# Optimization experiments

Hardware: AMD Instinct MI355X
Metric: run time of the kernel (lower is better)

## Reference

```python
import jax, jax.numpy as jnp
import numpy as np

HIDDEN = 512
HEADS = 8
HEAD_DIM = HIDDEN // HEADS  # 64
NUM_FEATURES = 256
EPS = 1e-4


def _gaussian_orthogonal_random_matrix(num_rows, num_cols, scaling=0, seed=1234):
    """Blocks of orthogonal rows from QR of gaussian matrices, rescaled (FAVOR+)."""
    rng = np.random.default_rng(seed)
    blocks = []
    full_blocks = num_rows // num_cols
    for _ in range(full_blocks):
        q, _ = np.linalg.qr(rng.standard_normal((num_cols, num_cols)))
        blocks.append(q.T)
    rem = num_rows - full_blocks * num_cols
    if rem > 0:
        q, _ = np.linalg.qr(rng.standard_normal((num_cols, num_cols)))
        blocks.append(q.T[:rem])
    mat = np.concatenate(blocks, axis=0)  # [num_rows, num_cols]
    if scaling == 0:
        # row norms of a fresh gaussian matrix (chi-distributed multipliers)
        multiplier = np.linalg.norm(rng.standard_normal((num_rows, num_cols)), axis=1)
    else:
        multiplier = np.sqrt(num_cols) * np.ones(num_rows)
    return (multiplier[:, None] * mat).astype(np.float32)


def _split_heads(x, b):
    # [b, n, hidden] -> [b, h, n, head_dim]
    return x.reshape(b, -1, HEADS, HEAD_DIM).transpose(0, 2, 1, 3)


def _phi(data, proj):
    """Nonnegative softmax kernel feature map (FAVOR+).
    data: [b,h,n,d], proj: [m,d] -> [b,h,n,m]"""
    d = data.shape[-1]
    m = proj.shape[0]
    x = data * (d ** -0.25)
    dash = jnp.einsum('bhnd,md->bhnm', x, proj)
    diag = 0.5 * jnp.sum(x * x, axis=-1, keepdims=True)
    return (m ** -0.5) * jnp.exp(dash - diag) + EPS


def setup_inputs() -> dict:
    key = jax.random.key(0)
    ks = jax.random.split(key, 12)
    b, n = 2, 8192
    s = HIDDEN ** -0.5
    inp = {
        'query': jax.random.normal(ks[0], (b, n, HIDDEN), jnp.float32),
        'key':   jax.random.normal(ks[1], (b, n, HIDDEN), jnp.float32),
        'value': jax.random.normal(ks[2], (b, n, HIDDEN), jnp.float32),
        'WQ_w': jax.random.normal(ks[3], (HIDDEN, HIDDEN), jnp.float32) * s,
        'WQ_b': jnp.zeros((HIDDEN,), jnp.float32),
        'WK_w': jax.random.normal(ks[4], (HIDDEN, HIDDEN), jnp.float32) * s,
        'WK_b': jnp.zeros((HIDDEN,), jnp.float32),
        'WV_w': jax.random.normal(ks[5], (HIDDEN, HIDDEN), jnp.float32) * s,
        'WV_b': jnp.zeros((HIDDEN,), jnp.float32),
        'WO_w': jax.random.normal(ks[6], (HIDDEN, HIDDEN), jnp.float32) * s,
        'WO_b': jnp.zeros((HIDDEN,), jnp.float32),
        'proj': jnp.asarray(_gaussian_orthogonal_random_matrix(NUM_FEATURES, HEAD_DIM)),
    }
    return inp


def reference(query, key, value, WQ_w, WQ_b, WK_w, WK_b, WV_w, WV_b, WO_w, WO_b, proj):
    b = query.shape[0]
    # torch Linear: y = x @ W.T + b
    Q = _split_heads(jnp.einsum('bnd,ed->bne', query, WQ_w) + WQ_b, b)
    K = _split_heads(jnp.einsum('bnd,ed->bne', key,   WK_w) + WK_b, b)
    V = _split_heads(jnp.einsum('bnd,ed->bne', value, WV_w) + WV_b, b)

    Qp = _phi(Q, proj)  # [b,h,n,m]
    Kp = _phi(K, proj)  # [b,h,n,m]

    # denominator: Q' @ sum_n K'  -> [b,h,n,1]
    denom = jnp.einsum('bhnm,bhm->bhn', Qp, jnp.sum(Kp, axis=2))[..., None]
    # linear attention: Q' @ (K'^T V), O(n*m*d)
    ctx = jnp.einsum('bhnm,bhnd->bhmd', Kp, V)
    attn = jnp.einsum('bhnm,bhmd->bhnd', Qp, ctx) / denom

    # faithful to original: .view(batch, -1, hidden) directly on [b,h,n,d]
    attn = attn.reshape(b, -1, HIDDEN)
    return jnp.einsum('bnd,ed->bne', attn, WO_w) + WO_b
```

## Files before the change

### kernel.cpp

```cpp
#include <hip/hip_runtime.h>

typedef __attribute__((ext_vector_type(8))) _Float16 f16x8;
typedef __attribute__((ext_vector_type(4))) float f32x4;

#define S4 0.35355339059327373f

static __device__ __forceinline__ ushort f2h(float f) {
  return __builtin_bit_cast(ushort, (_Float16)f);
}

static __device__ __forceinline__ void gload16(const void* g, void* l) {
  __builtin_amdgcn_global_load_lds((const __attribute__((address_space(1))) void*)g,
                                   (__attribute__((address_space(3))) void*)l, 16, 0, 0);
}

static __device__ __forceinline__ void cvt_store8(ushort* dst, float4 a, float4 b) {
  f16x8 h;
  h[0] = (_Float16)a.x; h[1] = (_Float16)a.y; h[2] = (_Float16)a.z; h[3] = (_Float16)a.w;
  h[4] = (_Float16)b.x; h[5] = (_Float16)b.y; h[6] = (_Float16)b.z; h[7] = (_Float16)b.w;
  *(f16x8*)dst = h;
}

template<int BM, int BN, int WR, int WC, int EPI, int ZMODE, int DIAG, int AF32, int BF32>
__global__ __launch_bounds__(256) void gemm_bt(
    const void* __restrict__ Av, const void* __restrict__ Bv,
    const float* __restrict__ bias, ushort* __restrict__ Cb,
    float* __restrict__ Cf, const float* __restrict__ rv0,
    float* __restrict__ dg,
    int K, int ldA, int ldB, int ldC, int Mz,
    long sAz, long sBz, long sCz)
{
  constexpr int BK = 32;
  constexpr int WTM = BM / WR, WTN = BN / WC;
  constexpr int MI = WTM / 16, NI = WTN / 16;
  constexpr int LDSB = (BM + BN) * 64;

  __shared__ uint4 smem4[LDSB / 16];
  char* smem = (char*)smem4;
  ushort* As = (ushort*)smem;
  ushort* Bs = (ushort*)(smem + BM * 64);

  const int tid = threadIdx.x;
  const int l = tid & 63, w = tid >> 6;
  const int wr = w / WC, wc = w % WC;
  const int lr = l & 15, lk = l >> 4;
  const int tm = blockIdx.x * BM, tn = blockIdx.y * BN;
  const int z = blockIdx.z;

  const ushort* Ah = (const ushort*)Av;
  const ushort* Bh = (const ushort*)Bv;
  const float*  Af = (const float*)Av;
  const float*  Bf = (const float*)Bv;
  long aoff = 0, boff = 0;
  if (ZMODE == 0) { aoff = (long)z * sAz; boff = (long)z * sBz; }
  if (ZMODE == 2) { aoff = (long)z * sAz; boff = (long)(z >> 3) * sBz + (z & 7) * 64; }
  if (ZMODE == 3) {
    aoff = (long)(z & 15) * sAz + (long)(z >> 4) * 1024;
    boff = (long)(z & 15) * sBz + (long)(z >> 4) * 1024;
  }
  Ah += aoff; Bh += boff; Af += aoff; Bf += boff;
  const float* rv = (EPI == 6) ? (rv0 + (long)z * Mz) : nullptr;
  const long coff = (long)z * sCz;

  f32x4 acc[MI][NI];
#pragma unroll
  for (int i = 0; i < MI; ++i)
#pragma unroll
    for (int j = 0; j < NI; ++j) acc[i][j] = f32x4{0.f, 0.f, 0.f, 0.f};

  for (int k0 = 0; k0 < K; k0 += BK) {
    if constexpr (AF32) {
      const int ar = tid >> 1, ac = (tid & 1) * 16;
      const float* g = Af + (long)(tm + ar) * ldA + k0 + ac;
      float4 f0 = *(const float4*)(g);
      float4 f1 = *(const float4*)(g + 4);
      float4 f2 = *(const float4*)(g + 8);
      float4 f3 = *(const float4*)(g + 12);
      cvt_store8(As + ar * 32 + ac, f0, f1);
      cvt_store8(As + ar * 32 + ac + 8, f2, f3);
    } else {
      constexpr int AB = BM * 64;
#pragma unroll
      for (int s = 0; s < (AB + 4095) / 4096; ++s) {
        const int base = s * 4096 + w * 1024;
        if (base < AB) {
          const int idx = base + l * 16;
          gload16(Ah + (long)(tm + (idx >> 6)) * ldA + k0 + ((idx & 63) >> 1),
                  (char*)As + base);
        }
      }
    }
    if constexpr (BF32) {
      const int br = tid >> 1, bc = (tid & 1) * 16;
      const float* g = Bf + (long)(tn + br) * ldB + k0 + bc;
      float4 f0 = *(const float4*)(g);
      float4 f1 = *(const float4*)(g + 4);
      float4 f2 = *(const float4*)(g + 8);
      float4 f3 = *(const float4*)(g + 12);
      cvt_store8(Bs + br * 32 + bc, f0, f1);
      cvt_store8(Bs + br * 32 + bc + 8, f2, f3);
    } else {
      constexpr int BB = BN * 64;
#pragma unroll
      for (int s = 0; s < (BB + 4095) / 4096; ++s) {
        const int base = s * 4096 + w * 1024;
        if (base < BB) {
          const int idx = base + l * 16;
          gload16(Bh + (long)(tn + (idx >> 6)) * ldB + k0 + ((idx & 63) >> 1),
                  (char*)Bs + base);
        }
      }
    }
    __syncthreads();

    f16x8 af[MI], bfr[NI];
#pragma unroll
    for (int mi = 0; mi < MI; ++mi)
      af[mi] = *(const f16x8*)(As + (wr * WTM + mi * 16 + lr) * 32 + lk * 8);
#pragma unroll
    for (int ni = 0; ni < NI; ++ni)
      bfr[ni] = *(const f16x8*)(Bs + (wc * WTN + ni * 16 + lr) * 32 + lk * 8);
#pragma unroll
    for (int mi = 0; mi < MI; ++mi)
#pragma unroll
      for (int ni = 0; ni < NI; ++ni)
        acc[mi][ni] = __builtin_amdgcn_mfma_f32_16x16x32_f16(af[mi], bfr[ni], acc[mi][ni], 0, 0, 0);
    __syncthreads();
  }

#pragma unroll
  for (int mi = 0; mi < MI; ++mi) {
#pragma unroll
    for (int j = 0; j < 4; ++j) {
      const int row = tm + wr * WTM + mi * 16 + lk * 4 + j;
      float ds = 0.f;
#pragma unroll
      for (int ni = 0; ni < NI; ++ni) {
        const int col = tn + wc * WTN + ni * 16 + lr;
        float v = acc[mi][ni][j];
        if (EPI == 0 || EPI == 3) v += bias[col];
        if (EPI == 4) v += bias[row];
        if (EPI == 6) v = 0.0625f * __expf(v - rv[col]) + 1e-4f;
        if (DIAG) ds += v * v;
        if (EPI == 4) {
          const int b = col >> 13, nn = col & 8191;
          const int h = row >> 6, d = row & 63;
          Cb[(long)(b * 8 + h) * 655360 + (long)d * 8192 + nn] = f2h(v);
        } else if (EPI == 3 || EPI == 5) {
          Cf[coff + (long)row * ldC + col] = v;
        } else {
          Cb[coff + (long)row * ldC + col] = f2h(v);
        }
      }
      if (DIAG) {
        ds += __shfl_xor(ds, 1, 64);
        ds += __shfl_xor(ds, 2, 64);
        ds += __shfl_xor(ds, 4, 64);
        ds += __shfl_xor(ds, 8, 64);
        if (lr == 0) {
          const int b = row >> 13, nn = row & 8191;
          const int head = (tn + wc * WTN) >> 6;
          dg[(long)(b * 8 + head) * 8192 + nn] = 0.0625f * ds;
        }
      }
    }
  }
}

__global__ __launch_bounds__(256) void phiattn_k(
    const ushort* __restrict__ Qh, const ushort* __restrict__ pjh,
    const float* __restrict__ diagQ, const ushort* __restrict__ ctxb,
    ushort* __restrict__ attnR)
{
  const int bx = blockIdx.x, bh = blockIdx.y;
  const int b = bh >> 3, h = bh & 7;
  const int tm = bx * 64;
  const int tid = threadIdx.x, l = tid & 63, w = tid >> 6;
  const int lr = l & 15, lk = l >> 4;

  __shared__ char smem[46080];
  ushort* P  = (ushort*)smem;
  ushort* As = (ushort*)(smem + 33792);
  ushort* Bs = (ushort*)(smem + 37888);

  const ushort* QB = Qh + (long)b * 4194304 + h * 64;
  const float* rv = diagQ + (long)bh * 8192;

  for (int nh = 0; nh < 2; ++nh) {
    const ushort* PB = pjh + nh * 8192;
    f32x4 a2[8];
#pragma unroll
    for (int i = 0; i < 8; ++i) a2[i] = f32x4{0.f, 0.f, 0.f, 0.f};

    for (int k0 = 0; k0 < 64; k0 += 32) {
      {
        const int base = w * 1024;
        const int idx = base + l * 16;
        gload16(QB + (long)(tm + (idx >> 6)) * 512 + k0 + ((idx & 63) >> 1),
                (char*)As + base);
      }
#pragma unroll
      for (int s = 0; s < 2; ++s) {
        const int base = s * 4096 + w * 1024;
        const int idx = base + l * 16;
        gload16(PB + (long)(idx >> 6) * 64 + k0 + ((idx & 63) >> 1),
                (char*)Bs + base);
      }
      __syncthreads();
      f16x8 af = *(const f16x8*)(As + (w * 16 + lr) * 32 + lk * 8);
#pragma unroll
      for (int ni = 0; ni < 8; ++ni) {
        f16x8 bfr = *(const f16x8*)(Bs + (ni * 16 + lr) * 32 + lk * 8);
        a2[ni] = __builtin_amdgcn_mfma_f32_16x16x32_f16(af, bfr, a2[ni], 0, 0, 0);
      }
      __syncthreads();
    }
#pragma unroll
    for (int ni = 0; ni < 8; ++ni)
#pragma unroll
      for (int j = 0; j < 4; ++j) {
        const int row = w * 16 + lk * 4 + j;
        const int col = nh * 128 + ni * 16 + lr;
        const float vv = 0.0625f * __expf(a2[ni][j] - rv[tm + row]) + 1e-4f;
        P[row * 264 + col] = f2h(vv);
      }
  }
  __syncthreads();

  f32x4 acc[5];
#pragma unroll
  for (int i = 0; i < 5; ++i) acc[i] = f32x4{0.f, 0.f, 0.f, 0.f};

  const ushort* cb = ctxb + (long)bh * 20480;
  for (int k0 = 0; k0 < 256; k0 += 32) {
    f16x8 pa = *(const f16x8*)(P + (w * 16 + lr) * 264 + k0 + lk * 8);
#pragma unroll
    for (int ni = 0; ni < 5; ++ni) {
      f16x8 cf = *(const f16x8*)(cb + (long)(ni * 16 + lr) * 256 + k0 + lk * 8);
      acc[ni] = __builtin_amdgcn_mfma_f32_16x16x32_f16(pa, cf, acc[ni], 0, 0, 0);
    }
  }

  ushort* outb = attnR + (long)bh * 524288;
#pragma unroll
  for (int j = 0; j < 4; ++j) {
    const float dv = __shfl(acc[4][j], (l & 48), 64);
    const int row = tm + w * 16 + lk * 4 + j;
#pragma unroll
    for (int ni = 0; ni < 4; ++ni) {
      const int col = ni * 16 + lr;
      outb[(long)row * 64 + col] = f2h(acc[ni][j] / dv);
    }
  }
}

__global__ __launch_bounds__(256) void cvtall_k(
    const float* __restrict__ wq, const float* __restrict__ wk,
    const float* __restrict__ wv, const float* __restrict__ wo,
    const float* __restrict__ pj,
    ushort* __restrict__ wqh, ushort* __restrict__ wkh,
    ushort* __restrict__ wvh, ushort* __restrict__ woh,
    ushort* __restrict__ pjh)
{
  int i = blockIdx.x * 256 + threadIdx.x;
  const float* in; ushort* out; float scale = 1.f; int idx;
  if (i < 65536)       { in = wq; out = wqh; idx = i; }
  else if (i < 131072) { in = wk; out = wkh; idx = i - 65536; }
  else if (i < 196608) { in = wv; out = wvh; idx = i - 131072; }
  else if (i < 262144) { in = wo; out = woh; idx = i - 196608; }
  else if (i < 266240) { in = pj; out = pjh; idx = i - 262144; scale = S4; }
  else return;
  float4 v = ((const float4*)in)[idx];
  ushort4 o;
  o.x = f2h(v.x * scale); o.y = f2h(v.y * scale);
  o.z = f2h(v.z * scale); o.w = f2h(v.w * scale);
  ((ushort4*)out)[idx] = o;
}

__global__ __launch_bounds__(256) void vtpad_k(ushort* __restrict__ Vt) {
  const int i = blockIdx.x * 256 + threadIdx.x;
  const int bh = i >> 14, rem = i & 16383, r = rem >> 10, n8 = rem & 1023;
  const unsigned val = (r == 0) ? 0x3C003C00u : 0u;
  uint4 u; u.x = val; u.y = val; u.z = val; u.w = val;
  *(uint4*)(Vt + (long)bh * 655360 + (long)(64 + r) * 8192 + n8 * 8) = u;
}

__global__ __launch_bounds__(256) void ctxred_k(const float* __restrict__ cp,
                                                ushort* __restrict__ ctxb) {
  const int idx = blockIdx.x * 256 + threadIdx.x;
  const int bh = idx / 20480, rem = idx % 20480;
  float a = 0.f;
#pragma unroll
  for (int kc = 0; kc < 8; ++kc) a += cp[(long)(kc * 16 + bh) * 20480 + rem];
  ctxb[idx] = f2h(a);
}

extern "C" void kernel_launch(void* const* d_in, const int* in_sizes, int n_in,
                              void* d_out, int out_size, void* d_ws, size_t ws_size,
                              hipStream_t stream) {
  (void)in_sizes; (void)n_in; (void)out_size; (void)ws_size;
  const float* q  = (const float*)d_in[0];
  const float* k  = (const float*)d_in[1];
  const float* v  = (const float*)d_in[2];
  const float* wq = (const float*)d_in[3];
  const float* bq = (const float*)d_in[4];
  const float* wk = (const float*)d_in[5];
  const float* bk = (const float*)d_in[6];
  const float* wv = (const float*)d_in[7];
  const float* bv = (const float*)d_in[8];
  const float* wo = (const float*)d_in[9];
  const float* bo = (const float*)d_in[10];
  const float* pj = (const float*)d_in[11];

  char* ws = (char*)d_ws;
  ushort* attnR = (ushort*)(ws + 0);
  float*  cpart = (float*)(ws + 16777216);
  ushort* wqh   = (ushort*)(ws + 27262976);
  ushort* wkh   = (ushort*)(ws + 27787264);
  ushort* wvh   = (ushort*)(ws + 28311552);
  ushort* woh   = (ushort*)(ws + 28835840);
  ushort* pjh   = (ushort*)(ws + 29360128);
  ushort* Qh    = (ushort*)(ws + 29392896);
  ushort* Kh    = (ushort*)(ws + 46170112);
  ushort* Vt    = (ushort*)(ws + 62947328);
  ushort* KpT   = (ushort*)(ws + 83918848);
  float*  diagQ = (float*)(ws + 151027712);
  float*  diagK = (float*)(ws + 151552000);
  ushort* ctxb  = (ushort*)(ws + 152076288);

  cvtall_k<<<1040, 256, 0, stream>>>(wq, wk, wv, wo, pj, wqh, wkh, wvh, woh, pjh);
  vtpad_k<<<1024, 256, 0, stream>>>(Vt);

  gemm_bt<128,128,2,2,0,0,1,1,0><<<dim3(128,4,1), 256, 0, stream>>>(
      q, wqh, bq, Qh, nullptr, nullptr, diagQ, 512, 512, 512, 512, 0, 0L, 0L, 0L);
  gemm_bt<128,128,2,2,0,0,1,1,0><<<dim3(128,4,1), 256, 0, stream>>>(
      k, wkh, bk, Kh, nullptr, nullptr, diagK, 512, 512, 512, 512, 0, 0L, 0L, 0L);

  gemm_bt<128,128,2,2,4,0,0,0,1><<<dim3(4,128,1), 256, 0, stream>>>(
      wvh, v, bv, Vt, nullptr, nullptr, nullptr, 512, 512, 512, 0, 0, 0L, 0L, 0L);

  gemm_bt<128,128,2,2,6,2,0,0,0><<<dim3(2,64,16), 256, 0, stream>>>(
      pjh, Kh, nullptr, KpT, nullptr, diagK, nullptr, 64, 64, 512, 8192, 8192,
      0L, 4194304L, 2097152L);

  gemm_bt<80,128,1,4,5,3,0,0,0><<<dim3(1,2,128), 256, 0, stream>>>(
      Vt, KpT, nullptr, nullptr, cpart, nullptr, nullptr, 1024, 8192, 8192, 256, 0,
      655360L, 2097152L, 20480L);
  ctxred_k<<<1280, 256, 0, stream>>>(cpart, ctxb);

  phiattn_k<<<dim3(128,16), 256, 0, stream>>>(Qh, pjh, diagQ, ctxb, attnR);

  gemm_bt<128,128,2,2,3,0,0,0,0><<<dim3(128,4,1), 256, 0, stream>>>(
      attnR, woh, bo, nullptr, (float*)d_out, nullptr, nullptr, 512, 512, 512, 512, 0,
      0L, 0L, 0L);
}
```

Measured before the change: 210.9 us.

## Stage full projection and ctx tiles in padded LDS for phi-attention kernel

Rewrites the phiattn kernel to load the whole 256x64 projection matrix and the 64-row Q tile into padded shared memory once, then compute all 256 features in a single pass instead of two halves with k-chunked global_load_lds staging. The ctx matrix is also copied into padded LDS (reusing the projection region) rather than read straight from global memory inside the MFMA loop. This cuts the barrier count and uncoalesced global fragment reads. In exchange, shared memory grows to about 78KB per block, which may lower occupancy, and the accumulator array doubles in register use.

```diff
diff --git a/kernel.cpp b/kernel.cpp
--- a/kernel.cpp
+++ b/kernel.cpp
@@ -178,65 +178,73 @@
   const int tid = threadIdx.x, l = tid & 63, w = tid >> 6;
   const int lr = l & 15, lk = l >> 4;
 
-  __shared__ char smem[46080];
+  __shared__ uint4 smem4[4992];
+  char* smem = (char*)smem4;
   ushort* P  = (ushort*)smem;
-  ushort* As = (ushort*)(smem + 33792);
-  ushort* Bs = (ushort*)(smem + 37888);
+  ushort* Pj = (ushort*)(smem + 33792);
+  ushort* As = (ushort*)(smem + 70656);
+  ushort* Cs = (ushort*)(smem + 33792);
 
   const ushort* QB = Qh + (long)b * 4194304 + h * 64;
   const float* rv = diagQ + (long)bh * 8192;
 
-  for (int nh = 0; nh < 2; ++nh) {
-    const ushort* PB = pjh + nh * 8192;
-    f32x4 a2[8];
-#pragma unroll
-    for (int i = 0; i < 8; ++i) a2[i] = f32x4{0.f, 0.f, 0.f, 0.f};
-
-    for (int k0 = 0; k0 < 64; k0 += 32) {
-      {
-        const int base = w * 1024;
-        const int idx = base + l * 16;
-        gload16(QB + (long)(tm + (idx >> 6)) * 512 + k0 + ((idx & 63) >> 1),
-                (char*)As + base);
-      }
-#pragma unroll
-      for (int s = 0; s < 2; ++s) {
-        const int base = s * 4096 + w * 1024;
-        const int idx = base + l * 16;
-        gload16(PB + (long)(idx >> 6) * 64 + k0 + ((idx & 63) >> 1),
-                (char*)Bs + base);
-      }
-      __syncthreads();
-      f16x8 af = *(const f16x8*)(As + (w * 16 + lr) * 32 + lk * 8);
-#pragma unroll
-      for (int ni = 0; ni < 8; ++ni) {
-        f16x8 bfr = *(const f16x8*)(Bs + (ni * 16 + lr) * 32 + lk * 8);
-        a2[ni] = __builtin_amdgcn_mfma_f32_16x16x32_f16(af, bfr, a2[ni], 0, 0, 0);
-      }
-      __syncthreads();
-    }
-#pragma unroll
-    for (int ni = 0; ni < 8; ++ni)
-#pragma unroll
-      for (int j = 0; j < 4; ++j) {
-        const int row = w * 16 + lk * 4 + j;
-        const int col = nh * 128 + ni * 16 + lr;
-        const float vv = 0.0625f * __expf(a2[ni][j] - rv[tm + row]) + 1e-4f;
-        P[row * 264 + col] = f2h(vv);
-      }
+#pragma unroll
+  for (int it = 0; it < 8; ++it) {
+    const int g = it * 256 + tid;
+    const int row = g >> 3, colg = (g & 7) * 8;
+    *(uint4*)(Pj + row * 72 + colg) = *(const uint4*)(pjh + row * 64 + colg);
+  }
+#pragma unroll
+  for (int it = 0; it < 2; ++it) {
+    const int g = it * 256 + tid;
+    const int row = g >> 3, colg = (g & 7) * 8;
+    *(uint4*)(As + row * 72 + colg) = *(const uint4*)(QB + (long)(tm + row) * 512 + colg);
   }
   __syncthreads();
 
+  f32x4 a2[16];
+#pragma unroll
+  for (int i = 0; i < 16; ++i) a2[i] = f32x4{0.f, 0.f, 0.f, 0.f};
+  {
+    f16x8 af0 = *(const f16x8*)(As + (w * 16 + lr) * 72 + lk * 8);
+    f16x8 af1 = *(const f16x8*)(As + (w * 16 + lr) * 72 + 32 + lk * 8);
+#pragma unroll
+    for (int ni = 0; ni < 16; ++ni) {
+      f16x8 b0 = *(const f16x8*)(Pj + (ni * 16 + lr) * 72 + lk * 8);
+      f16x8 b1 = *(const f16x8*)(Pj + (ni * 16 + lr) * 72 + 32 + lk * 8);
+      a2[ni] = __builtin_amdgcn_mfma_f32_16x16x32_f16(af0, b0, a2[ni], 0, 0, 0);
+      a2[ni] = __builtin_amdgcn_mfma_f32_16x16x32_f16(af1, b1, a2[ni], 0, 0, 0);
+    }
+  }
+#pragma unroll
+  for (int ni = 0; ni < 16; ++ni)
+#pragma unroll
+    for (int j = 0; j < 4; ++j) {
+      const int row = w * 16 + lk * 4 + j;
+      const int col = ni * 16 + lr;
+      const float vv = 0.0625f * __expf(a2[ni][j] - rv[tm + row]) + 1e-4f;
+      P[row * 264 + col] = f2h(vv);
+    }
+  __syncthreads();
+
+#pragma unroll
+  for (int it = 0; it < 10; ++it) {
+    const int g = it * 256 + tid;
+    const int row = g >> 5, colg = (g & 31) * 8;
+    *(uint4*)(Cs + row * 264 + colg) =
+        *(const uint4*)(ctxb + (long)bh * 20480 + row * 256 + colg);
+  }
+  __syncthreads();
+
   f32x4 acc[5];
 #pragma unroll
   for (int i = 0; i < 5; ++i) acc[i] = f32x4{0.f, 0.f, 0.f, 0.f};
 
-  const ushort* cb = ctxb + (long)bh * 20480;
   for (int k0 = 0; k0 < 256; k0 += 32) {
     f16x8 pa = *(const f16x8*)(P + (w * 16 + lr) * 264 + k0 + lk * 8);
 #pragma unroll
     for (int ni = 0; ni < 5; ++ni) {
-      f16x8 cf = *(const f16x8*)(cb + (long)(ni * 16 + lr) * 256 + k0 + lk * 8);
+      f16x8 cf = *(const f16x8*)(Cs + (ni * 16 + lr) * 264 + k0 + lk * 8);
       acc[ni] = __builtin_amdgcn_mfma_f32_16x16x32_f16(pa, cf, acc[ni], 0, 0, 0);
     }
   }
```

Result: faster. 187.3 us (-11.2%).
